# Kernel optimization log

Measured on AMD Instinct MI355X. Metric: run time of the kernel, lower is better.

## Reference

```python
import math
import jax, jax.numpy as jnp
import numpy as np

B, N, D, H = 4, 2048, 512, 8
HD = D // H


def setup_inputs() -> dict:
    key = jax.random.key(0)
    ks = jax.random.split(key, 7)
    w_scale = 1.0 / math.sqrt(D)  # keep logits in a sane range (like default init)
    return {
        "q": jax.random.normal(ks[0], (B, N, D), dtype=jnp.float32),
        "mask": jax.random.randint(ks[1], (B, N), 0, 2) == 1,  # True = masked key
        "attn_bias": jax.random.normal(ks[2], (B, N, N), dtype=jnp.float32),
        "Wq": jax.random.normal(ks[3], (D, D), dtype=jnp.float32) * w_scale,
        "Wk": jax.random.normal(ks[4], (D, D), dtype=jnp.float32) * w_scale,
        "Wv": jax.random.normal(ks[5], (D, D), dtype=jnp.float32) * w_scale,
        "Wo": jax.random.normal(ks[6], (D, D), dtype=jnp.float32) * w_scale,
    }


def _heads(v):
    # [B, N, D] -> [H, B, N, HD]  (mirrors reshape + movedim(-2, 0))
    b, n, d = v.shape
    return v.reshape(b, n, H, HD).transpose(2, 0, 1, 3)


def reference(q, mask, attn_bias, Wq, Wk, Wv, Wo):
    # Linear projections (torch Linear: x @ W.T)
    qh = _heads(q @ Wq.T)
    kh = _heads(q @ Wk.T)   # self-attention: h defaults to q
    vh = _heads(q @ Wv.T)
    # scores: [H, B, Nq, Nk]
    scores = jnp.einsum("hbqd,hbkd->hbqk", qh, kh) / math.sqrt(HD)
    scores = scores + attn_bias[None]                     # broadcast over heads
    scores = jnp.where(mask[None, :, None, :], -jnp.inf, scores)
    attn = jax.nn.softmax(scores, axis=-1)
    out = jnp.einsum("hbqk,hbkd->hbqd", attn, vh)         # [H, B, Nq, HD]
    out = out.transpose(1, 2, 0, 3).reshape(q.shape[0], q.shape[1], D)
    return out @ Wo.T
```

## Files before the change

kernel.cpp:

```cpp
#include <hip/hip_runtime.h>
#include <stdint.h>


typedef __attribute__((ext_vector_type(8))) short short8;
typedef __attribute__((ext_vector_type(4))) short short4v;
typedef __attribute__((ext_vector_type(4))) float f32x4;

#define DEV static __device__ __forceinline__

constexpr int Bc = 4, Nc = 2048, Dc = 512, Hc = 8, HDc = 64;
constexpr int Mc = Bc * Nc;
constexpr int QKVNc = 3 * Dc;
constexpr float L2E = 1.44269504f;

DEV short bf16cast(float f) {
  return (short)__builtin_bit_cast(unsigned short, (__bf16)f);
}
DEV unsigned cvt_pk_bf16(float a, float b) {
  unsigned short lb = __builtin_bit_cast(unsigned short, (__bf16)a);
  unsigned short hb = __builtin_bit_cast(unsigned short, (__bf16)b);
  return (unsigned)lb | ((unsigned)hb << 16);
}
DEV unsigned pack_shorts(short a, short b) {
  return (unsigned)(unsigned short)a | ((unsigned)(unsigned short)b << 16);
}
DEV short8 cvt8(float4 a, float4 b) {
  union { short8 s; uint4 u; } r;
  r.u.x = cvt_pk_bf16(a.x, a.y); r.u.y = cvt_pk_bf16(a.z, a.w);
  r.u.z = cvt_pk_bf16(b.x, b.y); r.u.w = cvt_pk_bf16(b.z, b.w);
  return r.s;
}
DEV float fast_exp2(float x) {
#if __has_builtin(__builtin_amdgcn_exp2f)
  return __builtin_amdgcn_exp2f(x);
#else
  return exp2f(x);
#endif
}

__global__ void cvtw_kernel(const float* __restrict__ Wq, const float* __restrict__ Wk,
                            const float* __restrict__ Wv, const float* __restrict__ Wo,
                            short* __restrict__ Wqkv, short* __restrict__ Wob) {
  int which = blockIdx.x >> 8;
  int j = (blockIdx.x & 255) * 256 + threadIdx.x;
  const float* src = which == 0 ? Wq : which == 1 ? Wk : which == 2 ? Wv : Wo;
  short* dst = (which == 3) ? Wob : Wqkv + which * (Dc * Dc);
  float4 v = ((const float4*)src)[j];
  short4v o = { bf16cast(v.x), bf16cast(v.y), bf16cast(v.z), bf16cast(v.w) };
  ((short4v*)dst)[j] = o;
}

__global__ void maskprep_kernel(const void* __restrict__ mask, float* __restrict__ mf) {
  __shared__ int flag;
  if (threadIdx.x == 0) flag = 0;
  __syncthreads();
  const uchar4* m4 = (const uchar4*)mask;
  int acc = 0;
  for (int i = threadIdx.x; i < 2048; i += 1024) {
    uchar4 v = m4[i];
    acc |= (int)v.y | (int)v.z | (int)v.w;
  }
  if (acc) atomicOr(&flag, 1);
  __syncthreads();
  int isbyte = flag;
  for (int i = threadIdx.x; i < Bc * Nc; i += 1024) {
    int v = isbyte ? (int)((const unsigned char*)mask)[i] : ((const int*)mask)[i];
    mf[i] = v ? -1e30f : 0.0f;
  }
}

template<bool A_F32, bool OUT_F32>
__global__ __launch_bounds__(256, 2) void gemm_bt(const void* __restrict__ Av,
                                                  const short* __restrict__ Bm,
                                                  void* __restrict__ Cv,
                                                  int M, int N, int K,
                                                  int qcols, float cscale) {
  __shared__ __align__(16) short At[128 * 72];
  __shared__ __align__(16) short Bt[128 * 72];
  const int tid = threadIdx.x, lane = tid & 63, wv = tid >> 6;
  const int quad = lane >> 4, l16 = lane & 15;
  const int mbase = blockIdx.y * 128, nbase = blockIdx.x * 128;
  const int wr = (wv >> 1) * 64, wc = (wv & 1) * 64;
  const float scale = (nbase < qcols) ? cscale : 1.0f;
  f32x4 acc[4][4] = {};
  float4 apf[4][2]; short8 aph[4], bpre[4];
#pragma unroll
  for (int i = 0; i < 4; i++) {
    int flat = i * 256 + tid, row = flat >> 3, ch8 = (flat & 7) * 8;
    if (A_F32) {
      const float* Af = (const float*)Av;
      apf[i][0] = *(const float4*)&Af[(size_t)(mbase + row) * K + ch8];
      apf[i][1] = *(const float4*)&Af[(size_t)(mbase + row) * K + ch8 + 4];
    } else {
      aph[i] = *(const short8*)&((const short*)Av)[(size_t)(mbase + row) * K + ch8];
    }
    bpre[i] = *(const short8*)&Bm[(size_t)(nbase + row) * K + ch8];
  }
  for (int k0 = 0; k0 < K; k0 += 64) {
    __syncthreads();
#pragma unroll
    for (int i = 0; i < 4; i++) {
      int flat = i * 256 + tid, row = flat >> 3, ch8 = (flat & 7) * 8;
      *(short8*)&At[row * 72 + ch8] = A_F32 ? cvt8(apf[i][0], apf[i][1]) : aph[i];
      *(short8*)&Bt[row * 72 + ch8] = bpre[i];
    }
    if (k0 + 64 < K) {
#pragma unroll
      for (int i = 0; i < 4; i++) {
        int flat = i * 256 + tid, row = flat >> 3, ch8 = (flat & 7) * 8;
        if (A_F32) {
          const float* Af = (const float*)Av;
          apf[i][0] = *(const float4*)&Af[(size_t)(mbase + row) * K + k0 + 64 + ch8];
          apf[i][1] = *(const float4*)&Af[(size_t)(mbase + row) * K + k0 + 64 + ch8 + 4];
        } else {
          aph[i] = *(const short8*)&((const short*)Av)[(size_t)(mbase + row) * K + k0 + 64 + ch8];
        }
        bpre[i] = *(const short8*)&Bm[(size_t)(nbase + row) * K + k0 + 64 + ch8];
      }
    }
    __syncthreads();
#pragma unroll
    for (int s = 0; s < 2; s++) {
      short8 af[4], bf[4];
#pragma unroll
      for (int t = 0; t < 4; t++) {
        af[t] = *(short8*)&At[(wr + t * 16 + l16) * 72 + quad * 8 + s * 32];
        bf[t] = *(short8*)&Bt[(wc + t * 16 + l16) * 72 + quad * 8 + s * 32];
      }
#pragma unroll
      for (int mt = 0; mt < 4; mt++)
#pragma unroll
        for (int nt = 0; nt < 4; nt++)
          acc[mt][nt] = __builtin_amdgcn_mfma_f32_16x16x32_bf16(af[mt], bf[nt], acc[mt][nt], 0, 0, 0);
    }
  }
#pragma unroll
  for (int mt = 0; mt < 4; mt++)
#pragma unroll
    for (int nt = 0; nt < 4; nt++)
#pragma unroll
      for (int r = 0; r < 4; r++) {
        int row = mbase + wr + mt * 16 + quad * 4 + r;
        int col = nbase + wc + nt * 16 + l16;
        float v = acc[mt][nt][r] * scale;
        if (OUT_F32) ((float*)Cv)[(size_t)row * N + col] = v;
        else         ((short*)Cv)[(size_t)row * N + col] = bf16cast(v);
      }
}

__global__ __launch_bounds__(256, 4) void attn_kernel(const short* __restrict__ QKV,
                                                      const float* __restrict__ bias,
                                                      const float* __restrict__ maskf,
                                                      short* __restrict__ Aout) {
  __shared__ __align__(16) short Kt[64 * 72];
  __shared__ __align__(16) short Vt[64 * 72];
  __shared__ __align__(16) short Pt[4][16 * 72];
  __shared__ __align__(16) float mlds[Nc];
  const int tid = threadIdx.x, lane = tid & 63, wv = tid >> 6;
  const int quad = lane >> 4, l16 = lane & 15;
  const int qt = blockIdx.x & 31, h = (blockIdx.x >> 5) & 7, b = (int)(blockIdx.x >> 8);
  const int qrow0 = qt * 64;
  const int qglob = qrow0 + wv * 16 + l16;
  const float* biasrow = bias + ((size_t)b * Nc + qglob) * Nc;
  const float* mfb = maskf + b * Nc;

  ((float4*)mlds)[tid]       = ((const float4*)mfb)[tid];
  ((float4*)mlds)[tid + 256] = ((const float4*)mfb)[tid + 256];

  short8 qf[2];
  {
    const short* qp = QKV + (size_t)(b * Nc + qglob) * QKVNc + h * HDc + quad * 8;
    qf[0] = *(const short8*)qp;
    qf[1] = *(const short8*)(qp + 32);
  }

  const int vp = tid & 31, vq = tid >> 5;
  const int krow = tid >> 3, kch = (tid & 7) * 8;
  const short* Kbase = QKV + Dc + h * HDc;
  const short* Vbase = QKV + 2 * Dc + h * HDc;

  short8 kpre0, kpre1; short4v v0pre[2], v1pre[2]; float4 bpre[4];
  kpre0 = *(const short8*)&Kbase[(size_t)(b * Nc + krow) * QKVNc + kch];
  kpre1 = *(const short8*)&Kbase[(size_t)(b * Nc + krow + 32) * QKVNc + kch];
#pragma unroll
  for (int g = 0; g < 2; g++) {
    v0pre[g] = *(const short4v*)&Vbase[(size_t)(b * Nc + 2 * vp) * QKVNc + 4 * (vq + 8 * g)];
    v1pre[g] = *(const short4v*)&Vbase[(size_t)(b * Nc + 2 * vp + 1) * QKVNc + 4 * (vq + 8 * g)];
  }
#pragma unroll
  for (int t = 0; t < 4; t++) bpre[t] = *(const float4*)&biasrow[t * 16 + quad * 4];

  const short ONEB = (short)0x3F80;
  const short8 ones = { ONEB, ONEB, ONEB, ONEB, ONEB, ONEB, ONEB, ONEB };

  f32x4 oacc[4] = {};
  f32x4 sumacc = {};

  for (int kt = 0; kt < 32; kt++) {
    const int kb = kt * 64;
    const int kbn = ((kt + 1) & 31) * 64;
    __syncthreads();
    *(short8*)&Kt[krow * 72 + kch] = kpre0;
    *(short8*)&Kt[(krow + 32) * 72 + kch] = kpre1;
#pragma unroll
    for (int g = 0; g < 2; g++)
#pragma unroll
      for (int j = 0; j < 4; j++)
        *(unsigned*)&Vt[(4 * (vq + 8 * g) + j) * 72 + 2 * vp] = pack_shorts(v0pre[g][j], v1pre[g][j]);

    f32x4 sacc[4];
#pragma unroll
    for (int t = 0; t < 4; t++) {
      float4 mv = *(const float4*)&mlds[kb + t * 16 + quad * 4];
      sacc[t][0] = __builtin_fmaf(bpre[t].x, L2E, mv.x);
      sacc[t][1] = __builtin_fmaf(bpre[t].y, L2E, mv.y);
      sacc[t][2] = __builtin_fmaf(bpre[t].z, L2E, mv.z);
      sacc[t][3] = __builtin_fmaf(bpre[t].w, L2E, mv.w);
    }

    kpre0 = *(const short8*)&Kbase[(size_t)(b * Nc + kbn + krow) * QKVNc + kch];
    kpre1 = *(const short8*)&Kbase[(size_t)(b * Nc + kbn + krow + 32) * QKVNc + kch];
#pragma unroll
    for (int g = 0; g < 2; g++) {
      v0pre[g] = *(const short4v*)&Vbase[(size_t)(b * Nc + kbn + 2 * vp) * QKVNc + 4 * (vq + 8 * g)];
      v1pre[g] = *(const short4v*)&Vbase[(size_t)(b * Nc + kbn + 2 * vp + 1) * QKVNc + 4 * (vq + 8 * g)];
    }
#pragma unroll
    for (int t = 0; t < 4; t++) bpre[t] = *(const float4*)&biasrow[kbn + t * 16 + quad * 4];
    __syncthreads();

#pragma unroll
    for (int s = 0; s < 2; s++)
#pragma unroll
      for (int t = 0; t < 4; t++) {
        short8 kf = *(short8*)&Kt[(t * 16 + l16) * 72 + quad * 8 + s * 32];
        sacc[t] = __builtin_amdgcn_mfma_f32_16x16x32_bf16(kf, qf[s], sacc[t], 0, 0, 0);
      }

#pragma unroll
    for (int t = 0; t < 4; t++) {
      float p0 = fast_exp2(sacc[t][0]);
      float p1 = fast_exp2(sacc[t][1]);
      float p2 = fast_exp2(sacc[t][2]);
      float p3 = fast_exp2(sacc[t][3]);
      uint2 u = { cvt_pk_bf16(p0, p1), cvt_pk_bf16(p2, p3) };
      *(uint2*)&Pt[wv][l16 * 72 + t * 16 + quad * 4] = u;
    }

#pragma unroll
    for (int s = 0; s < 2; s++) {
      short8 pf = *(short8*)&Pt[wv][l16 * 72 + quad * 8 + s * 32];
      sumacc = __builtin_amdgcn_mfma_f32_16x16x32_bf16(pf, ones, sumacc, 0, 0, 0);
#pragma unroll
      for (int t = 0; t < 4; t++) {
        short8 vf = *(short8*)&Vt[(t * 16 + l16) * 72 + quad * 8 + s * 32];
        oacc[t] = __builtin_amdgcn_mfma_f32_16x16x32_bf16(pf, vf, oacc[t], 0, 0, 0);
      }
    }
  }

#pragma unroll
  for (int r = 0; r < 4; r++) {
    float inv = 1.0f / sumacc[r];
    int row = b * Nc + qrow0 + wv * 16 + quad * 4 + r;
#pragma unroll
    for (int t = 0; t < 4; t++)
      Aout[(size_t)row * Dc + h * HDc + t * 16 + l16] = bf16cast(oacc[t][r] * inv);
  }
}

extern "C" void kernel_launch(void* const* d_in, const int* in_sizes, int n_in,
                              void* d_out, int out_size, void* d_ws, size_t ws_size,
                              hipStream_t stream) {
  const float* q    = (const float*)d_in[0];
  const void*  mask = d_in[1];
  const float* bias = (const float*)d_in[2];
  const float* Wq   = (const float*)d_in[3];
  const float* Wk   = (const float*)d_in[4];
  const float* Wv   = (const float*)d_in[5];
  const float* Wo   = (const float*)d_in[6];
  float* out = (float*)d_out;

  char* ws = (char*)d_ws;
  short* Wqkv = (short*)ws;  ws += (size_t)QKVNc * Dc * 2;
  short* Wob  = (short*)ws;  ws += (size_t)Dc * Dc * 2;
  float* mf   = (float*)ws;  ws += (size_t)Bc * Nc * 4;
  short* QKV  = (short*)ws;  ws += (size_t)Mc * QKVNc * 2;
  short* aout = (short*)ws;  ws += (size_t)Mc * Dc * 2;

  cvtw_kernel<<<dim3(1024), dim3(256), 0, stream>>>(Wq, Wk, Wv, Wo, Wqkv, Wob);
  maskprep_kernel<<<dim3(1), dim3(1024), 0, stream>>>(mask, mf);

  gemm_bt<true, false><<<dim3(QKVNc / 128, Mc / 128), dim3(256), 0, stream>>>(
      (const void*)q, Wqkv, (void*)QKV, Mc, QKVNc, Dc, Dc, 0.125f * L2E);
  attn_kernel<<<dim3(Bc * Hc * 32), dim3(256), 0, stream>>>(QKV, bias, mf, aout);
  gemm_bt<false, true><<<dim3(Dc / 128, Mc / 128), dim3(256), 0, stream>>>(
      (const void*)aout, Wob, (void*)out, Mc, Dc, Dc, 0, 1.0f);
}
```

Measured before the change: 292.3 us.

## Double-buffer LDS tiles in GEMM and attention, widen attention blocks, fuse mask prep

The GEMM and attention kernels now keep two LDS buffers for K/V and A/B tiles, so each loop iteration needs one barrier instead of two. The attention kernel moves to 512-thread blocks covering 128 query rows, which halves redundant K/V tile loads per query and spreads the tile fill across more threads. Mask preprocessing is folded into the weight-conversion kernel as an extra block, removing one launch. In exchange, LDS use per block doubles, which may lower occupancy, and larger blocks mean fewer blocks in the grid.

```diff
diff --git a/kernel.cpp b/kernel.cpp
--- a/kernel.cpp
+++ b/kernel.cpp
@@ -40,7 +40,27 @@
 
 __global__ void cvtw_kernel(const float* __restrict__ Wq, const float* __restrict__ Wk,
                             const float* __restrict__ Wv, const float* __restrict__ Wo,
-                            short* __restrict__ Wqkv, short* __restrict__ Wob) {
+                            short* __restrict__ Wqkv, short* __restrict__ Wob,
+                            const void* __restrict__ mask, float* __restrict__ mf) {
+  if (blockIdx.x == 1024) {
+    __shared__ int flag;
+    if (threadIdx.x == 0) flag = 0;
+    __syncthreads();
+    const uchar4* m4 = (const uchar4*)mask;
+    int acc = 0;
+    for (int i = threadIdx.x; i < 2048; i += 256) {
+      uchar4 v = m4[i];
+      acc |= (int)v.y | (int)v.z | (int)v.w;
+    }
+    if (acc) atomicOr(&flag, 1);
+    __syncthreads();
+    int isbyte = flag;
+    for (int i = threadIdx.x; i < Bc * Nc; i += 256) {
+      int v = isbyte ? (int)((const unsigned char*)mask)[i] : ((const int*)mask)[i];
+      mf[i] = v ? -1e30f : 0.0f;
+    }
+    return;
+  }
   int which = blockIdx.x >> 8;
   int j = (blockIdx.x & 255) * 256 + threadIdx.x;
   const float* src = which == 0 ? Wq : which == 1 ? Wk : which == 2 ? Wv : Wo;
@@ -50,33 +70,14 @@
   ((short4v*)dst)[j] = o;
 }
 
-__global__ void maskprep_kernel(const void* __restrict__ mask, float* __restrict__ mf) {
-  __shared__ int flag;
-  if (threadIdx.x == 0) flag = 0;
-  __syncthreads();
-  const uchar4* m4 = (const uchar4*)mask;
-  int acc = 0;
-  for (int i = threadIdx.x; i < 2048; i += 1024) {
-    uchar4 v = m4[i];
-    acc |= (int)v.y | (int)v.z | (int)v.w;
-  }
-  if (acc) atomicOr(&flag, 1);
-  __syncthreads();
-  int isbyte = flag;
-  for (int i = threadIdx.x; i < Bc * Nc; i += 1024) {
-    int v = isbyte ? (int)((const unsigned char*)mask)[i] : ((const int*)mask)[i];
-    mf[i] = v ? -1e30f : 0.0f;
-  }
-}
-
 template<bool A_F32, bool OUT_F32>
 __global__ __launch_bounds__(256, 2) void gemm_bt(const void* __restrict__ Av,
                                                   const short* __restrict__ Bm,
                                                   void* __restrict__ Cv,
                                                   int M, int N, int K,
                                                   int qcols, float cscale) {
-  __shared__ __align__(16) short At[128 * 72];
-  __shared__ __align__(16) short Bt[128 * 72];
+  __shared__ __align__(16) short At[2][128 * 72];
+  __shared__ __align__(16) short Bt[2][128 * 72];
   const int tid = threadIdx.x, lane = tid & 63, wv = tid >> 6;
   const int quad = lane >> 4, l16 = lane & 15;
   const int mbase = blockIdx.y * 128, nbase = blockIdx.x * 128;
@@ -97,13 +98,14 @@
     bpre[i] = *(const short8*)&Bm[(size_t)(nbase + row) * K + ch8];
   }
   for (int k0 = 0; k0 < K; k0 += 64) {
-    __syncthreads();
+    const int cur = (k0 >> 6) & 1;
 #pragma unroll
     for (int i = 0; i < 4; i++) {
       int flat = i * 256 + tid, row = flat >> 3, ch8 = (flat & 7) * 8;
-      *(short8*)&At[row * 72 + ch8] = A_F32 ? cvt8(apf[i][0], apf[i][1]) : aph[i];
-      *(short8*)&Bt[row * 72 + ch8] = bpre[i];
-    }
+      *(short8*)&At[cur][row * 72 + ch8] = A_F32 ? cvt8(apf[i][0], apf[i][1]) : aph[i];
+      *(short8*)&Bt[cur][row * 72 + ch8] = bpre[i];
+    }
+    __syncthreads();
     if (k0 + 64 < K) {
 #pragma unroll
       for (int i = 0; i < 4; i++) {
@@ -118,14 +120,13 @@
         bpre[i] = *(const short8*)&Bm[(size_t)(nbase + row) * K + k0 + 64 + ch8];
       }
     }
-    __syncthreads();
 #pragma unroll
     for (int s = 0; s < 2; s++) {
       short8 af[4], bf[4];
 #pragma unroll
       for (int t = 0; t < 4; t++) {
-        af[t] = *(short8*)&At[(wr + t * 16 + l16) * 72 + quad * 8 + s * 32];
-        bf[t] = *(short8*)&Bt[(wc + t * 16 + l16) * 72 + quad * 8 + s * 32];
+        af[t] = *(short8*)&At[cur][(wr + t * 16 + l16) * 72 + quad * 8 + s * 32];
+        bf[t] = *(short8*)&Bt[cur][(wc + t * 16 + l16) * 72 + quad * 8 + s * 32];
       }
 #pragma unroll
       for (int mt = 0; mt < 4; mt++)
@@ -148,24 +149,23 @@
       }
 }
 
-__global__ __launch_bounds__(256, 4) void attn_kernel(const short* __restrict__ QKV,
+__global__ __launch_bounds__(512, 2) void attn_kernel(const short* __restrict__ QKV,
                                                       const float* __restrict__ bias,
                                                       const float* __restrict__ maskf,
                                                       short* __restrict__ Aout) {
-  __shared__ __align__(16) short Kt[64 * 72];
-  __shared__ __align__(16) short Vt[64 * 72];
-  __shared__ __align__(16) short Pt[4][16 * 72];
+  __shared__ __align__(16) short Kt[2][64 * 72];
+  __shared__ __align__(16) short Vt[2][64 * 72];
+  __shared__ __align__(16) short Pt[8][16 * 72];
   __shared__ __align__(16) float mlds[Nc];
   const int tid = threadIdx.x, lane = tid & 63, wv = tid >> 6;
   const int quad = lane >> 4, l16 = lane & 15;
-  const int qt = blockIdx.x & 31, h = (blockIdx.x >> 5) & 7, b = (int)(blockIdx.x >> 8);
-  const int qrow0 = qt * 64;
+  const int qt = blockIdx.x & 15, h = (blockIdx.x >> 4) & 7, b = (int)(blockIdx.x >> 7);
+  const int qrow0 = qt * 128;
   const int qglob = qrow0 + wv * 16 + l16;
   const float* biasrow = bias + ((size_t)b * Nc + qglob) * Nc;
   const float* mfb = maskf + b * Nc;
 
-  ((float4*)mlds)[tid]       = ((const float4*)mfb)[tid];
-  ((float4*)mlds)[tid + 256] = ((const float4*)mfb)[tid + 256];
+  ((float4*)mlds)[tid] = ((const float4*)mfb)[tid];
 
   short8 qf[2];
   {
@@ -179,14 +179,10 @@
   const short* Kbase = QKV + Dc + h * HDc;
   const short* Vbase = QKV + 2 * Dc + h * HDc;
 
-  short8 kpre0, kpre1; short4v v0pre[2], v1pre[2]; float4 bpre[4];
-  kpre0 = *(const short8*)&Kbase[(size_t)(b * Nc + krow) * QKVNc + kch];
-  kpre1 = *(const short8*)&Kbase[(size_t)(b * Nc + krow + 32) * QKVNc + kch];
-#pragma unroll
-  for (int g = 0; g < 2; g++) {
-    v0pre[g] = *(const short4v*)&Vbase[(size_t)(b * Nc + 2 * vp) * QKVNc + 4 * (vq + 8 * g)];
-    v1pre[g] = *(const short4v*)&Vbase[(size_t)(b * Nc + 2 * vp + 1) * QKVNc + 4 * (vq + 8 * g)];
-  }
+  short8 kpre; short4v v0pre, v1pre; float4 bpre[4];
+  kpre  = *(const short8*)&Kbase[(size_t)(b * Nc + krow) * QKVNc + kch];
+  v0pre = *(const short4v*)&Vbase[(size_t)(b * Nc + 2 * vp) * QKVNc + 4 * vq];
+  v1pre = *(const short4v*)&Vbase[(size_t)(b * Nc + 2 * vp + 1) * QKVNc + 4 * vq];
 #pragma unroll
   for (int t = 0; t < 4; t++) bpre[t] = *(const float4*)&biasrow[t * 16 + quad * 4];
 
@@ -197,43 +193,41 @@
   f32x4 sumacc = {};
 
   for (int kt = 0; kt < 32; kt++) {
+    const int cur = kt & 1;
     const int kb = kt * 64;
     const int kbn = ((kt + 1) & 31) * 64;
-    __syncthreads();
-    *(short8*)&Kt[krow * 72 + kch] = kpre0;
-    *(short8*)&Kt[(krow + 32) * 72 + kch] = kpre1;
-#pragma unroll
-    for (int g = 0; g < 2; g++)
-#pragma unroll
-      for (int j = 0; j < 4; j++)
-        *(unsigned*)&Vt[(4 * (vq + 8 * g) + j) * 72 + 2 * vp] = pack_shorts(v0pre[g][j], v1pre[g][j]);
+
+    *(short8*)&Kt[cur][krow * 72 + kch] = kpre;
+#pragma unroll
+    for (int j = 0; j < 4; j++)
+      *(unsigned*)&Vt[cur][(4 * vq + j) * 72 + 2 * vp] = pack_shorts(v0pre[j], v1pre[j]);
+
+    __syncthreads();
+
+    float4 bcur[4];
+#pragma unroll
+    for (int t = 0; t < 4; t++) bcur[t] = bpre[t];
+    kpre  = *(const short8*)&Kbase[(size_t)(b * Nc + kbn + krow) * QKVNc + kch];
+    v0pre = *(const short4v*)&Vbase[(size_t)(b * Nc + kbn + 2 * vp) * QKVNc + 4 * vq];
+    v1pre = *(const short4v*)&Vbase[(size_t)(b * Nc + kbn + 2 * vp + 1) * QKVNc + 4 * vq];
+#pragma unroll
+    for (int t = 0; t < 4; t++) bpre[t] = *(const float4*)&biasrow[kbn + t * 16 + quad * 4];
 
     f32x4 sacc[4];
 #pragma unroll
     for (int t = 0; t < 4; t++) {
       float4 mv = *(const float4*)&mlds[kb + t * 16 + quad * 4];
-      sacc[t][0] = __builtin_fmaf(bpre[t].x, L2E, mv.x);
-      sacc[t][1] = __builtin_fmaf(bpre[t].y, L2E, mv.y);
-      sacc[t][2] = __builtin_fmaf(bpre[t].z, L2E, mv.z);
-      sacc[t][3] = __builtin_fmaf(bpre[t].w, L2E, mv.w);
-    }
-
-    kpre0 = *(const short8*)&Kbase[(size_t)(b * Nc + kbn + krow) * QKVNc + kch];
-    kpre1 = *(const short8*)&Kbase[(size_t)(b * Nc + kbn + krow + 32) * QKVNc + kch];
-#pragma unroll
-    for (int g = 0; g < 2; g++) {
-      v0pre[g] = *(const short4v*)&Vbase[(size_t)(b * Nc + kbn + 2 * vp) * QKVNc + 4 * (vq + 8 * g)];
-      v1pre[g] = *(const short4v*)&Vbase[(size_t)(b * Nc + kbn + 2 * vp + 1) * QKVNc + 4 * (vq + 8 * g)];
-    }
-#pragma unroll
-    for (int t = 0; t < 4; t++) bpre[t] = *(const float4*)&biasrow[kbn + t * 16 + quad * 4];
-    __syncthreads();
+      sacc[t][0] = __builtin_fmaf(bcur[t].x, L2E, mv.x);
+      sacc[t][1] = __builtin_fmaf(bcur[t].y, L2E, mv.y);
+      sacc[t][2] = __builtin_fmaf(bcur[t].z, L2E, mv.z);
+      sacc[t][3] = __builtin_fmaf(bcur[t].w, L2E, mv.w);
+    }
 
 #pragma unroll
     for (int s = 0; s < 2; s++)
 #pragma unroll
       for (int t = 0; t < 4; t++) {
-        short8 kf = *(short8*)&Kt[(t * 16 + l16) * 72 + quad * 8 + s * 32];
+        short8 kf = *(short8*)&Kt[cur][(t * 16 + l16) * 72 + quad * 8 + s * 32];
         sacc[t] = __builtin_amdgcn_mfma_f32_16x16x32_bf16(kf, qf[s], sacc[t], 0, 0, 0);
       }
 
@@ -253,7 +247,7 @@
       sumacc = __builtin_amdgcn_mfma_f32_16x16x32_bf16(pf, ones, sumacc, 0, 0, 0);
 #pragma unroll
       for (int t = 0; t < 4; t++) {
-        short8 vf = *(short8*)&Vt[(t * 16 + l16) * 72 + quad * 8 + s * 32];
+        short8 vf = *(short8*)&Vt[cur][(t * 16 + l16) * 72 + quad * 8 + s * 32];
         oacc[t] = __builtin_amdgcn_mfma_f32_16x16x32_bf16(pf, vf, oacc[t], 0, 0, 0);
       }
     }
@@ -288,12 +282,11 @@
   short* QKV  = (short*)ws;  ws += (size_t)Mc * QKVNc * 2;
   short* aout = (short*)ws;  ws += (size_t)Mc * Dc * 2;
 
-  cvtw_kernel<<<dim3(1024), dim3(256), 0, stream>>>(Wq, Wk, Wv, Wo, Wqkv, Wob);
-  maskprep_kernel<<<dim3(1), dim3(1024), 0, stream>>>(mask, mf);
+  cvtw_kernel<<<dim3(1025), dim3(256), 0, stream>>>(Wq, Wk, Wv, Wo, Wqkv, Wob, mask, mf);
 
   gemm_bt<true, false><<<dim3(QKVNc / 128, Mc / 128), dim3(256), 0, stream>>>(
       (const void*)q, Wqkv, (void*)QKV, Mc, QKVNc, Dc, Dc, 0.125f * L2E);
-  attn_kernel<<<dim3(Bc * Hc * 32), dim3(256), 0, stream>>>(QKV, bias, mf, aout);
+  attn_kernel<<<dim3(Bc * Hc * 16), dim3(512), 0, stream>>>(QKV, bias, mf, aout);
   gemm_bt<false, true><<<dim3(Dc / 128, Mc / 128), dim3(256), 0, stream>>>(
       (const void*)aout, Wob, (void*)out, Mc, Dc, Dc, 0, 1.0f);
 }
```

Result: faster. 277.6 us (-5.0%).
